# Optimization experiments

Hardware: AMD Instinct MI355X
Metric: run time of the kernel (lower is better)

The kernel has to match this reference:

```python
import jax, jax.numpy as jnp
import numpy as np
import math

B, T, O, D, H, L, FF = 2, 1024, 512, 1024, 16, 4, 4096
MAX_SEQ = 1024


def _ln(x, g, b, eps=1e-5):
    m = jnp.mean(x, -1, keepdims=True)
    v = jnp.mean((x - m) ** 2, -1, keepdims=True)
    return (x - m) * jax.lax.rsqrt(v + eps) * g + b


def _gelu(x):
    return jax.nn.gelu(x, approximate=False)  # torch nn.GELU default = exact erf


def setup_inputs() -> dict:
    key = jax.random.key(0)
    ks = iter(jax.random.split(key, 64))
    std = 0.02
    def w(shape):
        return (jax.random.normal(next(ks), shape, jnp.float32) * std)
    d = {
        'obs': jax.random.normal(next(ks), (B, T, O), jnp.float32),
        # encoder MLP: Linear(O,D), LN, GELU, Linear(D,D), GELU, Linear(D,D), LN
        'enc_w1': w((O, D)), 'enc_b1': jnp.zeros((D,)),
        'enc_g1': jnp.ones((D,)), 'enc_be1': jnp.zeros((D,)),
        'enc_w2': w((D, D)), 'enc_b2': jnp.zeros((D,)),
        'enc_w3': w((D, D)), 'enc_b3': jnp.zeros((D,)),
        'enc_g2': jnp.ones((D,)), 'enc_be2': jnp.zeros((D,)),
        'pos_emb': w((MAX_SEQ, D)),
        # stacked per-layer transformer params [L, ...]
        'ln1_g': jnp.ones((L, D)), 'ln1_b': jnp.zeros((L, D)),
        'wq': w((L, D, D)), 'bq': jnp.zeros((L, D)),
        'wk': w((L, D, D)), 'bk': jnp.zeros((L, D)),
        'wv': w((L, D, D)), 'bv': jnp.zeros((L, D)),
        'wo': w((L, D, D)), 'bo': jnp.zeros((L, D)),
        'ln2_g': jnp.ones((L, D)), 'ln2_b': jnp.zeros((L, D)),
        'mlp_w1': w((L, D, FF)), 'mlp_b1': jnp.zeros((L, FF)),
        'mlp_w2': w((L, FF, D)), 'mlp_b2': jnp.zeros((L, D)),
        'lnf_g': jnp.ones((D,)), 'lnf_b': jnp.zeros((D,)),
        'dec_w': w((D, O)), 'dec_b': jnp.zeros((O,)),
    }
    return d


def reference(obs, enc_w1, enc_b1, enc_g1, enc_be1, enc_w2, enc_b2, enc_w3, enc_b3,
              enc_g2, enc_be2, pos_emb, ln1_g, ln1_b, wq, bq, wk, bk, wv, bv, wo, bo,
              ln2_g, ln2_b, mlp_w1, mlp_b1, mlp_w2, mlp_b2, lnf_g, lnf_b, dec_w, dec_b):
    b, t, _ = obs.shape
    dh = D // H
    scale = 1.0 / math.sqrt(dh)
    # embedder MLP
    h = _gelu(_ln(obs @ enc_w1 + enc_b1, enc_g1, enc_be1))
    h = _gelu(h @ enc_w2 + enc_b2)
    h = _ln(h @ enc_w3 + enc_b3, enc_g2, enc_be2)
    x = h + pos_emb[:t]
    # causal mask [t, t]
    mask = jnp.tril(jnp.ones((t, t), bool))

    def block(x, p):
        g1, b1, Wq, Bq, Wk, Bk, Wv, Bv, Wo, Bo, g2, b2, W1, B1, W2, B2 = p
        hn = _ln(x, g1, b1)
        q = (hn @ Wq + Bq).reshape(b, t, H, dh).transpose(0, 2, 1, 3)
        k = (hn @ Wk + Bk).reshape(b, t, H, dh).transpose(0, 2, 1, 3)
        v = (hn @ Wv + Bv).reshape(b, t, H, dh).transpose(0, 2, 1, 3)
        att = jnp.einsum('bhtd,bhsd->bhts', q, k) * scale
        att = jnp.where(mask, att, -jnp.inf)
        att = jax.nn.softmax(att, axis=-1)
        y = jnp.einsum('bhts,bhsd->bhtd', att, v)
        y = y.transpose(0, 2, 1, 3).reshape(b, t, D)
        x = x + y @ Wo + Bo
        hm = _ln(x, g2, b2)
        x = x + _gelu(hm @ W1 + B1) @ W2 + B2
        return x, None

    stacked = (ln1_g, ln1_b, wq, bq, wk, bk, wv, bv, wo, bo,
               ln2_g, ln2_b, mlp_w1, mlp_b1, mlp_w2, mlp_b2)
    x, _ = jax.lax.scan(block, x, stacked)
    x = _ln(x, lnf_g, lnf_b)
    out_obs = x @ dec_w + dec_b
    return x, out_obs
```

## Files before the change

kernel.cpp:

```cpp
#include <hip/hip_runtime.h>
#include <utility>

typedef unsigned short u16;
typedef __bf16  bf16x8 __attribute__((ext_vector_type(8)));
typedef float   f32x4  __attribute__((ext_vector_type(4)));
typedef unsigned short u16x4 __attribute__((ext_vector_type(4)));

constexpr int Bc = 2, Tc = 1024, Oc = 512, Dc = 1024, Hc = 16, Lc = 4, FFc = 4096;
constexpr int Mc = Bc * Tc;
constexpr int Sq = 3 * Dc;

__device__ __forceinline__ u16 f2b(float f) {
    unsigned u = __float_as_uint(f);
    u = (u + 0x7fffu + ((u >> 16) & 1u)) >> 16;
    return (u16)u;
}
__device__ __forceinline__ float gelu_f(float x) {
    return 0.5f * x * (1.0f + erff(x * 0.7071067811865476f));
}

__global__ __launch_bounds__(256) void wtrans(const float* __restrict__ in,
                                              u16* __restrict__ out, int R, int C,
                                              long inBatch, long outBatch) {
    __shared__ float t[32][33];
    const float* inp = in + (size_t)blockIdx.z * inBatch;
    u16* outp = out + (size_t)blockIdx.z * outBatch;
    const int tx = threadIdx.x & 31, ty = threadIdx.x >> 5;
    const int br = blockIdx.y * 32, bc = blockIdx.x * 32;
#pragma unroll
    for (int i = 0; i < 32; i += 8)
        t[ty + i][tx] = inp[(size_t)(br + ty + i) * C + bc + tx];
    __syncthreads();
#pragma unroll
    for (int i = 0; i < 32; i += 8)
        outp[(size_t)(bc + ty + i) * R + br + tx] = f2b(t[tx][ty + i]);
}

__global__ __launch_bounds__(256) void btrans(const u16* __restrict__ in,
                                              u16* __restrict__ out, int inStride) {
    __shared__ u16 t[32][33];
    const u16* inp = in + (size_t)blockIdx.z * Tc * inStride;
    u16* outp = out + (size_t)blockIdx.z * Dc * Tc;
    const int tx = threadIdx.x & 31, ty = threadIdx.x >> 5;
    const int br = blockIdx.y * 32, bc = blockIdx.x * 32;
#pragma unroll
    for (int i = 0; i < 32; i += 8)
        t[ty + i][tx] = inp[(size_t)(br + ty + i) * inStride + bc + tx];
    __syncthreads();
#pragma unroll
    for (int i = 0; i < 32; i += 8)
        outp[(size_t)(bc + ty + i) * Tc + br + tx] = t[tx][ty + i];
}

__global__ __launch_bounds__(256) void cvt_bf(const float* __restrict__ in,
                                              u16* __restrict__ out, int n) {
    int i = blockIdx.x * 256 + threadIdx.x;
    if (i * 4 >= n) return;
    float4 v = ((const float4*)in)[i];
    u16x4 r;
    r[0] = f2b(v.x); r[1] = f2b(v.y); r[2] = f2b(v.z); r[3] = f2b(v.w);
    ((u16x4*)out)[i] = r;
}

__global__ __launch_bounds__(256) void pack_qkv_bias(const float* __restrict__ bq,
    const float* __restrict__ bk, const float* __restrict__ bv, float* __restrict__ out) {
    int i = blockIdx.x * 256 + threadIdx.x;
    int l = i / Sq, j = i % Sq;
    float v = (j < Dc) ? bq[l * Dc + j] : (j < 2 * Dc ? bk[l * Dc + j - Dc] : bv[l * Dc + j - 2 * Dc]);
    out[i] = v;
}

__global__ __launch_bounds__(256) void red2(const float* __restrict__ p,
    const float* __restrict__ bias, const float* __restrict__ resid,
    float* __restrict__ outf, int MN) {
    const int i = blockIdx.x * 256 + threadIdx.x;
    const f32x4 a = ((const f32x4*)p)[i];
    const f32x4 b = ((const f32x4*)(p + MN))[i];
    const int col4 = i & (Dc / 4 - 1);
    const f32x4 bb = ((const f32x4*)bias)[col4];
    const f32x4 r  = ((const f32x4*)resid)[i];
    f32x4 o;
#pragma unroll
    for (int j = 0; j < 4; ++j) o[j] = a[j] + b[j] + bb[j] + r[j];
    ((f32x4*)outf)[i] = o;
}

__global__ __launch_bounds__(256) void ln_kernel(
    const float* __restrict__ in, const float* __restrict__ gam,
    const float* __restrict__ bet, const float* __restrict__ pos,
    float* __restrict__ outf, u16* __restrict__ outb, int do_gelu) {
    const int row = blockIdx.x, tid = threadIdx.x;
    const float4 v = ((const float4*)(in + (size_t)row * Dc))[tid];
    float s  = v.x + v.y + v.z + v.w;
    float ss = v.x * v.x + v.y * v.y + v.z * v.z + v.w * v.w;
#pragma unroll
    for (int m = 1; m < 64; m <<= 1) {
        s  += __shfl_xor(s,  m, 64);
        ss += __shfl_xor(ss, m, 64);
    }
    __shared__ float red[8];
    const int w = tid >> 6;
    if ((tid & 63) == 0) { red[w] = s; red[4 + w] = ss; }
    __syncthreads();
    s  = red[0] + red[1] + red[2] + red[3];
    ss = red[4] + red[5] + red[6] + red[7];
    const float mean = s * (1.0f / Dc);
    const float rstd = rsqrtf(ss * (1.0f / Dc) - mean * mean + 1e-5f);
    const float4 gv = ((const float4*)gam)[tid];
    const float4 bv = ((const float4*)bet)[tid];
    float y0 = (v.x - mean) * rstd * gv.x + bv.x;
    float y1 = (v.y - mean) * rstd * gv.y + bv.y;
    float y2 = (v.z - mean) * rstd * gv.z + bv.z;
    float y3 = (v.w - mean) * rstd * gv.w + bv.w;
    if (do_gelu) { y0 = gelu_f(y0); y1 = gelu_f(y1); y2 = gelu_f(y2); y3 = gelu_f(y3); }
    if (pos) {
        const float4 pv = ((const float4*)(pos + (size_t)(row & (Tc - 1)) * Dc))[tid];
        y0 += pv.x; y1 += pv.y; y2 += pv.z; y3 += pv.w;
    }
    if (outf) {
        float4 o; o.x = y0; o.y = y1; o.z = y2; o.w = y3;
        ((float4*)(outf + (size_t)row * Dc))[tid] = o;
    }
    if (outb) {
        u16x4 r; r[0] = f2b(y0); r[1] = f2b(y1); r[2] = f2b(y2); r[3] = f2b(y3);
        ((u16x4*)(outb + (size_t)row * Dc))[tid] = r;
    }
}

template<int BM, int BN, int FM, int FN, int WM, int WN, int OCC>
__global__ __launch_bounds__(256, OCC) void gemm_k(
    const u16* __restrict__ A, const u16* __restrict__ Bt,
    const float* __restrict__ bias, const float* resid,
    float* Cf, u16* Cb, int M, int N, int Kst, int Kl, int do_gelu) {
    __shared__ u16 sA[2][BM][64];
    __shared__ u16 sB[2][BN][64];
    constexpr int NA = BM * 8 / 256;
    constexpr int NB = BN * 8 / 256;
    const int tid = threadIdx.x;
    const int lane = tid & 63, w = tid >> 6;
    const int lr = lane & 15, g = lane >> 4;
    const int wm = w / WN, wn = w % WN;

    A  += (size_t)blockIdx.z * Kl;
    Bt += (size_t)blockIdx.z * Kl;
    Cf += (size_t)blockIdx.z * M * N;

    const int gx = gridDim.x;
    const int nwg = gx * gridDim.y;
    const int orig = blockIdx.y * gx + blockIdx.x;
    const int wgid = (orig & 7) * (nwg >> 3) + (orig >> 3);
    const int s = wgid >> 6, q = wgid & 63;
    const int nsx = gx >> 3;
    const int sy = s / nsx, sx = s - sy * nsx;
    const int by = sy * 8 + (q >> 3), bx = sx * 8 + (q & 7);
    const long m0 = (long)by * BM, n0 = (long)bx * BN;

    const f32x4 fzero = {0.f, 0.f, 0.f, 0.f};
    f32x4 acc[FM][FN];
#pragma unroll
    for (int i = 0; i < FM; ++i)
#pragma unroll
        for (int j = 0; j < FN; ++j) acc[i][j] = fzero;

    const int nt = Kl / 64;
    bf16x8 ra[2][NA], rb[2][NB];

    const u16* gA[NA];
    const u16* gB[NB];
#pragma unroll
    for (int i = 0; i < NA; ++i) {
        int c = tid + 256 * i, row = c >> 3, cc = c & 7;
        gA[i] = A + (size_t)(m0 + row) * Kst + cc * 8;
    }
#pragma unroll
    for (int i = 0; i < NB; ++i) {
        int c = tid + 256 * i, row = c >> 3, cc = c & 7;
        gB[i] = Bt + (size_t)(n0 + row) * Kst + cc * 8;
    }

    auto gload = [&](auto curc, int t) {
        constexpr int cu = decltype(curc)::value;
        if (t < nt) {
#pragma unroll
            for (int i = 0; i < NA; ++i) { ra[cu][i] = *(const bf16x8*)gA[i]; gA[i] += 64; }
#pragma unroll
            for (int i = 0; i < NB; ++i) { rb[cu][i] = *(const bf16x8*)gB[i]; gB[i] += 64; }
        }
    };
    auto lwrite = [&](auto curc) {
        constexpr int cu = decltype(curc)::value;
#pragma unroll
        for (int i = 0; i < NA; ++i) {
            int c = tid + 256 * i, row = c >> 3, cc = c & 7;
            *(bf16x8*)&sA[cu][row][(cc ^ (row & 7)) * 8] = ra[cu][i];
        }
#pragma unroll
        for (int i = 0; i < NB; ++i) {
            int c = tid + 256 * i, row = c >> 3, cc = c & 7;
            *(bf16x8*)&sB[cu][row][(cc ^ (row & 7)) * 8] = rb[cu][i];
        }
    };
    auto compute = [&](auto curc) {
        constexpr int cu = decltype(curc)::value;
#pragma unroll
        for (int ks = 0; ks < 2; ++ks) {
            bf16x8 fa[FM], fb[FN];
#pragma unroll
            for (int mi = 0; mi < FM; ++mi) {
                int row = wm * (16 * FM) + mi * 16 + lr;
                fa[mi] = *(const bf16x8*)&sA[cu][row][((ks * 4 + g) ^ (row & 7)) * 8];
            }
#pragma unroll
            for (int ni = 0; ni < FN; ++ni) {
                int row = wn * (16 * FN) + ni * 16 + lr;
                fb[ni] = *(const bf16x8*)&sB[cu][row][((ks * 4 + g) ^ (row & 7)) * 8];
            }
#pragma unroll
            for (int mi = 0; mi < FM; ++mi)
#pragma unroll
                for (int ni = 0; ni < FN; ++ni)
                    acc[mi][ni] = __builtin_amdgcn_mfma_f32_16x16x32_bf16(
                        fa[mi], fb[ni], acc[mi][ni], 0, 0, 0);
        }
    };

    std::integral_constant<int, 0> c0;
    std::integral_constant<int, 1> c1;
    gload(c0, 0);
    gload(c1, 1);
    lwrite(c0);
    __syncthreads();
    for (int t = 0; t < nt; t += 2) {
        gload(c0, t + 2);
        compute(c0);
        lwrite(c1);
        __syncthreads();
        gload(c1, t + 3);
        compute(c1);
        if (t + 2 < nt) {
            lwrite(c0);
            __syncthreads();
        }
    }
#pragma unroll
    for (int mi = 0; mi < FM; ++mi) {
#pragma unroll
        for (int ni = 0; ni < FN; ++ni) {
            const long nc = n0 + wn * (16 * FN) + ni * 16 + lr;
            const float bvv = bias ? bias[nc] : 0.0f;
#pragma unroll
            for (int j = 0; j < 4; ++j) {
                const long mr = m0 + wm * (16 * FM) + mi * 16 + g * 4 + j;
                float v = acc[mi][ni][j] + bvv;
                if (resid) v += resid[(size_t)mr * N + nc];
                if (do_gelu) v = gelu_f(v);
                if (Cf) Cf[(size_t)mr * N + nc] = v;
                if (Cb) Cb[(size_t)mr * N + nc] = f2b(v);
            }
        }
    }
}

__global__ __launch_bounds__(256, 2) void attn_kernel(
    const u16* __restrict__ qkv, const u16* __restrict__ Vt, u16* __restrict__ Yg) {
    __shared__ u16 sK[64][64];
    __shared__ u16 sV[64][64];
    __shared__ u16 sP[4][16][64];
    const int tid = threadIdx.x, w = tid >> 6, lane = tid & 63;
    const int lr = lane & 15, g = lane >> 4;
    const int hw = blockIdx.x;
    const int xcd = hw & 7, slot = hw >> 3;
    const int bh = xcd + 8 * (slot >> 4);
    const int qc = slot & 15;
    const int h = bh & 15, b = bh >> 4;
    const int tq0 = qc * 64 + w * 16;
    const u16* Qp = qkv + (size_t)b * Tc * Sq + h * 64;
    const u16* Kp = qkv + (size_t)b * Tc * Sq + Dc + h * 64;
    const u16* Vp = Vt + ((size_t)b * Dc + h * 64) * Tc;

    bf16x8 qf[2];
#pragma unroll
    for (int ks = 0; ks < 2; ++ks)
        qf[ks] = *(const bf16x8*)(Qp + (size_t)(tq0 + lr) * Sq + ks * 32 + g * 8);

    const f32x4 fzero = {0.f, 0.f, 0.f, 0.f};
    f32x4 o[4];
    float mst[4], lst[4];
#pragma unroll
    for (int j = 0; j < 4; ++j) { mst[j] = -1e30f; lst[j] = 0.f; }
#pragma unroll
    for (int ni = 0; ni < 4; ++ni) o[ni] = fzero;

    for (int jk = 0; jk <= qc; ++jk) {
#pragma unroll
        for (int i = 0; i < 2; ++i) {
            int c = tid + 256 * i;
            int row = c >> 3, cc = c & 7;
            *(bf16x8*)&sK[row][(cc ^ (row & 7)) * 8] =
                *(const bf16x8*)(Kp + (size_t)(jk * 64 + row) * Sq + cc * 8);
            *(bf16x8*)&sV[row][(cc ^ (row & 7)) * 8] =
                *(const bf16x8*)(Vp + (size_t)row * Tc + jk * 64 + cc * 8);
        }
        __syncthreads();
        f32x4 s[4];
#pragma unroll
        for (int ni = 0; ni < 4; ++ni) {
            const int row = ni * 16 + lr;
            bf16x8 kf0 = *(const bf16x8*)&sK[row][((0 + g) ^ (lr & 7)) * 8];
            bf16x8 kf1 = *(const bf16x8*)&sK[row][((4 + g) ^ (lr & 7)) * 8];
            s[ni] = __builtin_amdgcn_mfma_f32_16x16x32_bf16(qf[0], kf0, fzero, 0, 0, 0);
            s[ni] = __builtin_amdgcn_mfma_f32_16x16x32_bf16(qf[1], kf1, s[ni], 0, 0, 0);
        }
#pragma unroll
        for (int ni = 0; ni < 4; ++ni)
#pragma unroll
            for (int j = 0; j < 4; ++j) {
                float v = s[ni][j] * 0.125f;
                int tk = jk * 64 + ni * 16 + lr;
                int tq = tq0 + g * 4 + j;
                if (tk > tq) v = -1e30f;
                s[ni][j] = v;
            }
        float fs[4];
#pragma unroll
        for (int j = 0; j < 4; ++j) {
            float pm = fmaxf(fmaxf(s[0][j], s[1][j]), fmaxf(s[2][j], s[3][j]));
            pm = fmaxf(pm, __shfl_xor(pm, 1, 16));
            pm = fmaxf(pm, __shfl_xor(pm, 2, 16));
            pm = fmaxf(pm, __shfl_xor(pm, 4, 16));
            pm = fmaxf(pm, __shfl_xor(pm, 8, 16));
            const float m2 = fmaxf(mst[j], pm);
            fs[j] = __expf(mst[j] - m2);
#pragma unroll
            for (int ni = 0; ni < 4; ++ni)
                s[ni][j] = __expf(s[ni][j] - m2);
            float rsum = s[0][j] + s[1][j] + s[2][j] + s[3][j];
            rsum += __shfl_xor(rsum, 1, 16);
            rsum += __shfl_xor(rsum, 2, 16);
            rsum += __shfl_xor(rsum, 4, 16);
            rsum += __shfl_xor(rsum, 8, 16);
            lst[j] = lst[j] * fs[j] + rsum;
            mst[j] = m2;
        }
#pragma unroll
        for (int ni = 0; ni < 4; ++ni)
#pragma unroll
            for (int j = 0; j < 4; ++j) o[ni][j] *= fs[j];
#pragma unroll
        for (int ni = 0; ni < 4; ++ni)
#pragma unroll
            for (int j = 0; j < 4; ++j) {
                int row = g * 4 + j;
                int col = ni * 16 + lr;
                sP[w][row][(((col >> 3) ^ (row & 7)) << 3) | (col & 7)] = f2b(s[ni][j]);
            }
#pragma unroll
        for (int ks = 0; ks < 2; ++ks) {
            bf16x8 pf = *(const bf16x8*)&sP[w][lr][((ks * 4 + g) ^ (lr & 7)) * 8];
#pragma unroll
            for (int ni = 0; ni < 4; ++ni) {
                const int row = ni * 16 + lr;
                bf16x8 vf = *(const bf16x8*)&sV[row][((ks * 4 + g) ^ (lr & 7)) * 8];
                o[ni] = __builtin_amdgcn_mfma_f32_16x16x32_bf16(pf, vf, o[ni], 0, 0, 0);
            }
        }
        __syncthreads();
    }
#pragma unroll
    for (int ni = 0; ni < 4; ++ni)
#pragma unroll
        for (int j = 0; j < 4; ++j) {
            int tq = tq0 + g * 4 + j;
            int col = h * 64 + ni * 16 + lr;
            Yg[(size_t)(b * Tc + tq) * Dc + col] = f2b(o[ni][j] / lst[j]);
        }
}

extern "C" void kernel_launch(void* const* d_in, const int* in_sizes, int n_in,
                              void* d_out, int out_size, void* d_ws, size_t ws_size,
                              hipStream_t stream) {
    const float* obs    = (const float*)d_in[0];
    const float* enc_w1 = (const float*)d_in[1];
    const float* enc_b1 = (const float*)d_in[2];
    const float* enc_g1 = (const float*)d_in[3];
    const float* enc_be1= (const float*)d_in[4];
    const float* enc_w2 = (const float*)d_in[5];
    const float* enc_b2 = (const float*)d_in[6];
    const float* enc_w3 = (const float*)d_in[7];
    const float* enc_b3 = (const float*)d_in[8];
    const float* enc_g2 = (const float*)d_in[9];
    const float* enc_be2= (const float*)d_in[10];
    const float* pos_emb= (const float*)d_in[11];
    const float* ln1_g  = (const float*)d_in[12];
    const float* ln1_b  = (const float*)d_in[13];
    const float* wq     = (const float*)d_in[14];
    const float* bq     = (const float*)d_in[15];
    const float* wk     = (const float*)d_in[16];
    const float* bk     = (const float*)d_in[17];
    const float* wv     = (const float*)d_in[18];
    const float* bv     = (const float*)d_in[19];
    const float* wo     = (const float*)d_in[20];
    const float* bo     = (const float*)d_in[21];
    const float* ln2_g  = (const float*)d_in[22];
    const float* ln2_b  = (const float*)d_in[23];
    const float* mlp_w1 = (const float*)d_in[24];
    const float* mlp_b1 = (const float*)d_in[25];
    const float* mlp_w2 = (const float*)d_in[26];
    const float* mlp_b2 = (const float*)d_in[27];
    const float* lnf_g  = (const float*)d_in[28];
    const float* lnf_b  = (const float*)d_in[29];
    const float* dec_w  = (const float*)d_in[30];
    const float* dec_b  = (const float*)d_in[31];

    float* out_x = (float*)d_out;
    float* out_o = out_x + (size_t)Mc * Dc;

    char* base = (char*)d_ws;
    size_t off = 0;
    auto ab = [&](size_t e) -> u16* {
        u16* r = (u16*)(base + off); off += (e * 2 + 255) & ~(size_t)255; return r; };
    auto af = [&](size_t e) -> float* {
        float* r = (float*)(base + off); off += (e * 4 + 255) & ~(size_t)255; return r; };

    u16* wt_e1   = ab((size_t)Dc * Oc);
    u16* wt_e2   = ab((size_t)Dc * Dc);
    u16* wt_e3   = ab((size_t)Dc * Dc);
    u16* wtqkv   = ab((size_t)Lc * 3 * Dc * Dc);
    u16* wto     = ab((size_t)Lc * Dc * Dc);
    u16* wtm1    = ab((size_t)Lc * Dc * FFc);
    u16* wtm2    = ab((size_t)Lc * FFc * Dc);
    u16* wt_d    = ab((size_t)Oc * Dc);
    float* qkvb  = af((size_t)Lc * Sq);

    u16*   obs_bf = ab((size_t)Mc * Oc);
    float* tmpf   = af((size_t)Mc * Dc);
    float* xf     = af((size_t)Mc * Dc);
    float* x2f    = af((size_t)Mc * Dc);
    u16*   hn_bf  = ab((size_t)Mc * Dc);
    u16*   qkv    = ab((size_t)Mc * Sq);
    u16*   vT     = ab((size_t)Mc * Dc);
    u16*   y_bf   = ab((size_t)Mc * Dc);
    u16*   ff_bf  = ab((size_t)Mc * FFc);
    float* pk     = af((size_t)2 * Mc * Dc);

    wtrans<<<dim3(Dc / 32, Oc / 32, 1), 256, 0, stream>>>(enc_w1, wt_e1, Oc, Dc, 0, 0);
    wtrans<<<dim3(Dc / 32, Dc / 32, 1), 256, 0, stream>>>(enc_w2, wt_e2, Dc, Dc, 0, 0);
    wtrans<<<dim3(Dc / 32, Dc / 32, 1), 256, 0, stream>>>(enc_w3, wt_e3, Dc, Dc, 0, 0);
    wtrans<<<dim3(Dc / 32, Dc / 32, Lc), 256, 0, stream>>>(wq, wtqkv,            Dc, Dc, (long)Dc * Dc, (long)3 * Dc * Dc);
    wtrans<<<dim3(Dc / 32, Dc / 32, Lc), 256, 0, stream>>>(wk, wtqkv + Dc * Dc,  Dc, Dc, (long)Dc * Dc, (long)3 * Dc * Dc);
    wtrans<<<dim3(Dc / 32, Dc / 32, Lc), 256, 0, stream>>>(wv, wtqkv + 2 * Dc * Dc, Dc, Dc, (long)Dc * Dc, (long)3 * Dc * Dc);
    wtrans<<<dim3(Dc / 32, Dc / 32, Lc), 256, 0, stream>>>(wo, wto, Dc, Dc, (long)Dc * Dc, (long)Dc * Dc);
    wtrans<<<dim3(FFc / 32, Dc / 32, Lc), 256, 0, stream>>>(mlp_w1, wtm1, Dc, FFc, (long)Dc * FFc, (long)Dc * FFc);
    wtrans<<<dim3(Dc / 32, FFc / 32, Lc), 256, 0, stream>>>(mlp_w2, wtm2, FFc, Dc, (long)Dc * FFc, (long)Dc * FFc);
    wtrans<<<dim3(Oc / 32, Dc / 32, 1), 256, 0, stream>>>(dec_w, wt_d, Dc, Oc, 0, 0);
    pack_qkv_bias<<<dim3(Lc * Sq / 256), 256, 0, stream>>>(bq, bk, bv, qkvb);
    cvt_bf<<<dim3((Mc * Oc / 4 + 255) / 256), 256, 0, stream>>>(obs, obs_bf, Mc * Oc);

    auto g128 = [&](const u16* A, const u16* Bt, const float* bias, const float* resid,
                    float* Cf, u16* Cb, int M, int N, int K, int gel) {
        gemm_k<128, 128, 4, 4, 2, 2, 2><<<dim3(N / 128, M / 128), 256, 0, stream>>>(
            A, Bt, bias, resid, Cf, Cb, M, N, K, K, gel);
    };
    auto g64 = [&](const u16* A, const u16* Bt, const float* bias, const float* resid,
                   float* Cf, u16* Cb, int M, int N, int K, int gel) {
        gemm_k<64, 64, 2, 2, 2, 2, 4><<<dim3(N / 64, M / 64), 256, 0, stream>>>(
            A, Bt, bias, resid, Cf, Cb, M, N, K, K, gel);
    };
    auto lnk = [&](const float* in, const float* gg, const float* bb, const float* pos,
                   float* outf, u16* outb, int gel) {
        ln_kernel<<<dim3(Mc), 256, 0, stream>>>(in, gg, bb, pos, outf, outb, gel);
    };

    g64(obs_bf, wt_e1, enc_b1, nullptr, tmpf, nullptr, Mc, Dc, Oc, 0);
    lnk(tmpf, enc_g1, enc_be1, nullptr, nullptr, hn_bf, 1);
    g64(hn_bf, wt_e2, enc_b2, nullptr, nullptr, y_bf, Mc, Dc, Dc, 1);
    g64(y_bf, wt_e3, enc_b3, nullptr, tmpf, nullptr, Mc, Dc, Dc, 0);
    lnk(tmpf, enc_g2, enc_be2, pos_emb, xf, nullptr, 0);

    for (int l = 0; l < Lc; ++l) {
        lnk(xf, ln1_g + (size_t)l * Dc, ln1_b + (size_t)l * Dc, nullptr, nullptr, hn_bf, 0);
        g128(hn_bf, wtqkv + (size_t)l * 3 * Dc * Dc, qkvb + (size_t)l * Sq, nullptr,
             nullptr, qkv, Mc, Sq, Dc, 0);
        btrans<<<dim3(Dc / 32, Tc / 32, Bc), 256, 0, stream>>>(qkv + 2 * Dc, vT, Sq);
        attn_kernel<<<dim3(Bc * Hc * (Tc / 64)), 256, 0, stream>>>(qkv, vT, y_bf);
        g64(y_bf, wto + (size_t)l * Dc * Dc, bo + (size_t)l * Dc, xf, x2f, nullptr, Mc, Dc, Dc, 0);
        lnk(x2f, ln2_g + (size_t)l * Dc, ln2_b + (size_t)l * Dc, nullptr, nullptr, hn_bf, 0);
        g128(hn_bf, wtm1 + (size_t)l * Dc * FFc, mlp_b1 + (size_t)l * FFc, nullptr,
             nullptr, ff_bf, Mc, FFc, Dc, 1);
        gemm_k<64, 64, 2, 2, 2, 2, 4><<<dim3(Dc / 64, Mc / 64, 2), 256, 0, stream>>>(
            ff_bf, wtm2 + (size_t)l * FFc * Dc, nullptr, nullptr, pk, nullptr,
            Mc, Dc, FFc, FFc / 2, 0);
        red2<<<dim3(Mc * Dc / 4 / 256), 256, 0, stream>>>(
            pk, mlp_b2 + (size_t)l * Dc, x2f, xf, Mc * Dc);
    }

    lnk(xf, lnf_g, lnf_b, nullptr, out_x, hn_bf, 0);
    g64(hn_bf, wt_d, dec_b, nullptr, out_o, nullptr, Mc, Oc, Dc, 0);
}
```

Measured before the change: 793.8 us.

## Load GEMM tiles directly into LDS with global_load_lds instead of register staging

```diff
diff --git a/kernel.cpp b/kernel.cpp
--- a/kernel.cpp
+++ b/kernel.cpp
@@ -17,6 +17,12 @@
 }
 __device__ __forceinline__ float gelu_f(float x) {
     return 0.5f * x * (1.0f + erff(x * 0.7071067811865476f));
+}
+
+typedef const __attribute__((address_space(1))) void* gas_p;
+typedef __attribute__((address_space(3))) void* las_p;
+__device__ __forceinline__ void gload16(const void* g, void* l) {
+    __builtin_amdgcn_global_load_lds((gas_p)g, (las_p)l, 16, 0, 0);
 }
 
 __global__ __launch_bounds__(256) void wtrans(const float* __restrict__ in,
@@ -134,8 +140,8 @@
     float* Cf, u16* Cb, int M, int N, int Kst, int Kl, int do_gelu) {
     __shared__ u16 sA[2][BM][64];
     __shared__ u16 sB[2][BN][64];
-    constexpr int NA = BM * 8 / 256;
-    constexpr int NB = BN * 8 / 256;
+    constexpr int NA = BM / 32;
+    constexpr int NB = BN / 32;
     const int tid = threadIdx.x;
     const int lane = tid & 63, w = tid >> 6;
     const int lr = lane & 15, g = lane >> 4;
@@ -163,41 +169,23 @@
         for (int j = 0; j < FN; ++j) acc[i][j] = fzero;
 
     const int nt = Kl / 64;
-    bf16x8 ra[2][NA], rb[2][NB];
-
-    const u16* gA[NA];
-    const u16* gB[NB];
-#pragma unroll
-    for (int i = 0; i < NA; ++i) {
-        int c = tid + 256 * i, row = c >> 3, cc = c & 7;
-        gA[i] = A + (size_t)(m0 + row) * Kst + cc * 8;
-    }
-#pragma unroll
-    for (int i = 0; i < NB; ++i) {
-        int c = tid + 256 * i, row = c >> 3, cc = c & 7;
-        gB[i] = Bt + (size_t)(n0 + row) * Kst + cc * 8;
-    }
-
-    auto gload = [&](auto curc, int t) {
+    const int srow = lane >> 3, scc = lane & 7;
+    const u16* pa[NA];
+    const u16* pb[NB];
+#pragma unroll
+    for (int r = 0; r < NA; ++r)
+        pa[r] = A + (size_t)(m0 + r * 32 + w * 8 + srow) * Kst + ((scc ^ srow) * 8);
+#pragma unroll
+    for (int r = 0; r < NB; ++r)
+        pb[r] = Bt + (size_t)(n0 + r * 32 + w * 8 + srow) * Kst + ((scc ^ srow) * 8);
+
+    auto stage = [&](auto curc, int t) {
         constexpr int cu = decltype(curc)::value;
         if (t < nt) {
 #pragma unroll
-            for (int i = 0; i < NA; ++i) { ra[cu][i] = *(const bf16x8*)gA[i]; gA[i] += 64; }
-#pragma unroll
-            for (int i = 0; i < NB; ++i) { rb[cu][i] = *(const bf16x8*)gB[i]; gB[i] += 64; }
-        }
-    };
-    auto lwrite = [&](auto curc) {
-        constexpr int cu = decltype(curc)::value;
-#pragma unroll
-        for (int i = 0; i < NA; ++i) {
-            int c = tid + 256 * i, row = c >> 3, cc = c & 7;
-            *(bf16x8*)&sA[cu][row][(cc ^ (row & 7)) * 8] = ra[cu][i];
-        }
-#pragma unroll
-        for (int i = 0; i < NB; ++i) {
-            int c = tid + 256 * i, row = c >> 3, cc = c & 7;
-            *(bf16x8*)&sB[cu][row][(cc ^ (row & 7)) * 8] = rb[cu][i];
+            for (int r = 0; r < NA; ++r) { gload16(pa[r], &sA[cu][r * 32 + w * 8][0]); pa[r] += 64; }
+#pragma unroll
+            for (int r = 0; r < NB; ++r) { gload16(pb[r], &sB[cu][r * 32 + w * 8][0]); pb[r] += 64; }
         }
     };
     auto compute = [&](auto curc) {
@@ -223,24 +211,23 @@
                         fa[mi], fb[ni], acc[mi][ni], 0, 0, 0);
         }
     };
+    auto drain_barrier = [&]() {
+        asm volatile("s_waitcnt vmcnt(0)" ::: "memory");
+        __builtin_amdgcn_sched_barrier(0);
+        __syncthreads();
+    };
 
     std::integral_constant<int, 0> c0;
     std::integral_constant<int, 1> c1;
-    gload(c0, 0);
-    gload(c1, 1);
-    lwrite(c0);
-    __syncthreads();
+    stage(c0, 0);
+    drain_barrier();
     for (int t = 0; t < nt; t += 2) {
-        gload(c0, t + 2);
+        stage(c1, t + 1);
         compute(c0);
-        lwrite(c1);
-        __syncthreads();
-        gload(c1, t + 3);
+        drain_barrier();
+        stage(c0, t + 2);
         compute(c1);
-        if (t + 2 < nt) {
-            lwrite(c0);
-            __syncthreads();
-        }
+        drain_barrier();
     }
 #pragma unroll
     for (int mi = 0; mi < FM; ++mi) {
```

After: 781.5 us. About the same (-1.5%).
